# Kernel optimization log

Hardware: AMD Instinct MI355X
Metric: run time of the kernel (lower is better)

Reference implementation:

```python
import jax, jax.numpy as jnp
import numpy as np

B, H, W = 16, 512, 512
N_BINS = 511          # round(mean(shape)) - 1 for (512, 512)
MAX_R = 1.0           # (1 + min(shape)/max(shape)) / 2 for square image


def _bin_ids():
    # Precompute per-pixel radial shell index (replaces the list of boolean shell masks).
    frame = max(H, W)
    xx, yy = np.mgrid[:H, :W]
    ellipse = ((xx - H / 2) * 2 / frame) ** 2 + ((yy - W / 2) * 2 / frame) ** 2
    r2 = np.linspace(0.0, MAX_R, N_BINS + 1)[1:] ** 2
    # shell k = { r2[k-1] <= ellipse < r2[k] }; pixels with ellipse >= r2[-1] map to
    # overflow bin N_BINS and are dropped, exactly matching the xor'd ellipse masks.
    return jnp.asarray(np.searchsorted(r2, ellipse.ravel(), side='right').astype(np.int32))


BIN_IDS = _bin_ids()  # [H*W] int32 in [0, N_BINS]


def setup_inputs() -> dict:
    key = jax.random.key(0)
    k1, k2 = jax.random.split(key)
    return {
        "z_": jax.random.normal(k1, (B, H, W, 2), dtype=jnp.float32),
        "t_": jax.random.normal(k2, (B, H, W, 2), dtype=jnp.float32),
    }


def _shell_sums(x):
    # x: [B, H*W] -> per-shell sums [B, N_BINS+1] in a single fused segment-sum pass.
    return jax.vmap(lambda v: jax.ops.segment_sum(v, BIN_IDS, num_segments=N_BINS + 1))(x)


def reference(z_, t_):
    tc = t_[..., 0] + 1j * t_[..., 1]          # [B,H,W] complex target
    zc = z_[..., 0] + 1j * z_[..., 1]
    Ft = jnp.fft.fft2(tc, axes=(-2, -1))
    Fe = jnp.fft.fft2(zc - tc, axes=(-2, -1))
    norm_coeff = Ft.real ** 2 + Ft.imag ** 2   # |FFT(target)|^2, [B,H,W]
    errors = Fe.real ** 2 + Fe.imag ** 2       # |FFT(z - target)|^2
    es = _shell_sums(errors.reshape(B, -1))[:, :N_BINS]      # drop overflow bin
    ns = _shell_sums(norm_coeff.reshape(B, -1))[:, :N_BINS]
    nre = es / jnp.maximum(ns, 1e-8)           # per-batch, per-shell normed error
    # per_shell_loss = per-batch sum over shells; loss = mean over batch
    return jnp.mean(jnp.sum(nre, axis=1))
```

## Files before the change

### kernel.cpp

```cpp
#include <hip/hip_runtime.h>

#define HH 512
#define WW 512
#define NBATCH 16
#define NBINS 512
#define NREP 8

#define PI_F 3.14159265358979323846f

#define SW(r) ((r) ^ (((r) >> 4) & 0xF))
#define TSW(c, hh) (((c) << 3) + ((hh) ^ (((c) >> 1) & 7)))

#define DPP_SHR(x, n) __builtin_amdgcn_update_dpp(0, (x), 0x110 + (n), 0xF, 0xF, true)
#define DPP_SHL1(x)   __builtin_amdgcn_update_dpp(0, (x), 0x101,       0xF, 0xF, true)

__device__ __forceinline__ float2 cadd(float2 a, float2 b){ return make_float2(a.x+b.x, a.y+b.y); }
__device__ __forceinline__ float2 csub(float2 a, float2 b){ return make_float2(a.x-b.x, a.y-b.y); }
__device__ __forceinline__ float2 cmul(float2 a, float2 b){
    return make_float2(a.x*b.x - a.y*b.y, a.x*b.y + a.y*b.x);
}

__device__ __forceinline__ void dft8(const float2* a, float2* y) {
    const float s2 = 0.70710678118654752440f;
    float2 t02a = cadd(a[0], a[4]), t02s = csub(a[0], a[4]);
    float2 t13a = cadd(a[2], a[6]), t13s = csub(a[2], a[6]);
    float2 E0 = cadd(t02a, t13a);
    float2 E2 = csub(t02a, t13a);
    float2 E1 = make_float2(t02s.x + t13s.y, t02s.y - t13s.x);
    float2 E3 = make_float2(t02s.x - t13s.y, t02s.y + t13s.x);
    float2 u02a = cadd(a[1], a[5]), u02s = csub(a[1], a[5]);
    float2 u13a = cadd(a[3], a[7]), u13s = csub(a[3], a[7]);
    float2 O0 = cadd(u02a, u13a);
    float2 O2 = csub(u02a, u13a);
    float2 O1 = make_float2(u02s.x + u13s.y, u02s.y - u13s.x);
    float2 O3 = make_float2(u02s.x - u13s.y, u02s.y + u13s.x);
    float2 wO1 = make_float2(s2 * (O1.x + O1.y), s2 * (O1.y - O1.x));
    float2 wO2 = make_float2(O2.y, -O2.x);
    float2 wO3 = make_float2(s2 * (O3.y - O3.x), -s2 * (O3.x + O3.y));
    y[0] = cadd(E0, O0);  y[4] = csub(E0, O0);
    y[1] = cadd(E1, wO1); y[5] = csub(E1, wO1);
    y[2] = cadd(E2, wO2); y[6] = csub(E2, wO2);
    y[3] = cadd(E3, wO3); y[7] = csub(E3, wO3);
}

__device__ __forceinline__ void twiddle8(float base, float2* w) {
    float s1, c1, s4, c4;
    __sincosf(base, &s1, &c1);
    __sincosf(4.0f * base, &s4, &c4);
    w[0] = make_float2(1.0f, 0.0f);
    w[1] = make_float2(c1, s1);
    w[2] = cmul(w[1], w[1]);
    w[3] = cmul(w[2], w[1]);
    w[4] = make_float2(c4, s4);
    w[5] = cmul(w[4], w[1]);
    w[6] = cmul(w[4], w[2]);
    w[7] = cmul(w[4], w[3]);
}

__device__ __forceinline__ void fft512_stage0_store(float2* rb, int lane, const float2* a) {
    float2 y[8]; dft8(a, y);
    float2 w[8]; twiddle8(-PI_F * (float)lane * (1.0f / 256.0f), w);
#pragma unroll
    for (int r = 0; r < 8; ++r) rb[SW(8 * lane + r)] = cmul(y[r], w[r]);
}

__device__ __forceinline__ void fft512_stage1(float2* rb, int lane) {
    float2 a[8];
#pragma unroll
    for (int u = 0; u < 8; ++u) a[u] = rb[SW(lane + 64 * u)];
    float2 y[8]; dft8(a, y);
    float2 w[8]; twiddle8(-PI_F * (float)(lane >> 3) * (1.0f / 32.0f), w);
    const int qb = (lane & 7) + ((lane >> 3) << 6);
#pragma unroll
    for (int r = 0; r < 8; ++r) rb[SW(qb + 8 * r)] = cmul(y[r], w[r]);
}

__device__ __forceinline__ void fft512_stage2(const float2* rb, int lane, float2* y) {
    float2 a[8];
#pragma unroll
    for (int u = 0; u < 8; ++u) a[u] = rb[SW(lane + 64 * u)];
    dft8(a, y);
}

__global__ __launch_bounds__(512, 4)
void row_fft_kernel(const float2* __restrict__ z, const float2* __restrict__ t,
                    float2* __restrict__ fieldsT, int b0) {
    __shared__ float2 buf[8 * 512];
    const int tid  = threadIdx.x;
    const int lane = tid & 63;
    const int g    = tid >> 6;
    const int bid  = blockIdx.x;
    const int hg   = bid & 63;
    const int lb   = bid >> 6;
    const int b    = b0 + lb;
    const int h    = (hg << 3) | g;
    const size_t rowOff = ((size_t)(b * HH + h)) * WW;

    const float2* tr = t + rowOff;
    const float2* zr = z + rowOff;
    float2 tv[8], zv[8];
#pragma unroll
    for (int u = 0; u < 8; ++u) tv[u] = tr[lane + 64 * u];
#pragma unroll
    for (int u = 0; u < 8; ++u) zv[u] = zr[lane + 64 * u];

    float2* rb = buf + (g << 9);
#pragma unroll
    for (int f = 0; f < 2; ++f) {
        float2 a[8];
        if (f == 0) {
#pragma unroll
            for (int u = 0; u < 8; ++u) a[u] = tv[u];
        } else {
#pragma unroll
            for (int u = 0; u < 8; ++u) a[u] = make_float2(zv[u].x - tv[u].x,
                                                           zv[u].y - tv[u].y);
        }
        fft512_stage0_store(rb, lane, a);
        __builtin_amdgcn_wave_barrier();
        fft512_stage1(rb, lane);
        __builtin_amdgcn_wave_barrier();
        float2 y[8];
        fft512_stage2(rb, lane, y);

        __syncthreads();
#pragma unroll
        for (int r = 0; r < 8; ++r) {
            int c = lane + (r << 6);
            buf[TSW(c, g)] = y[r];
        }
        __syncthreads();
        float2* outF = fieldsT + ((size_t)(lb * 2 + f) << 18);
#pragma unroll
        for (int k = 0; k < 8; ++k) {
            int e  = tid + (k << 9);
            int c  = e >> 3;
            int hh = e & 7;
            outF[((size_t)c << 9) + (hg << 3) + hh] = buf[TSW(c, hh)];
        }
        __syncthreads();
    }
}

__global__ __launch_bounds__(256, 8)
void col_fft_bin_kernel(const float2* __restrict__ fieldsT,
                        float* __restrict__ binsR, int b0) {
    __shared__ float2 buf[4 * 512];
    const int tid  = threadIdx.x;
    const int lane = tid & 63;
    const int g    = tid >> 6;
    const int bid  = blockIdx.x;
    const int cq   = bid & 127;
    const int f    = (bid >> 7) & 1;
    const int lb   = bid >> 8;
    const int b    = b0 + lb;
    const int c    = (cq << 2) | g;

    const float2* colT = fieldsT + (((size_t)(lb * 2 + f) << 9) + c) * 512;
    float2 a[8];
#pragma unroll
    for (int u = 0; u < 8; ++u) a[u] = colT[lane + (u << 6)];

    float2* rb = buf + (g << 9);
    fft512_stage0_store(rb, lane, a);
    __builtin_amdgcn_wave_barrier();
    fft512_stage1(rb, lane);
    __builtin_amdgcn_wave_barrier();
    float2 y[8];
    fft512_stage2(rb, lane, y);
    __builtin_amdgcn_wave_barrier();
    __asm__ volatile("" ::: "memory");

#pragma unroll
    for (int j = 0; j < 4; ++j) rb[lane + (j << 6)] = make_float2(0.0f, 0.0f);
    __builtin_amdgcn_wave_barrier();
    __asm__ volatile("" ::: "memory");

    float* histw = (float*)rb;
    const int dc = c - 256;
    const unsigned fc2i = (unsigned)(dc * dc);
    const int l15 = lane & 15;
#pragma unroll
    for (int r = 0; r < 8; ++r) {
        int k  = lane + (r << 6);
        int dk = k - 256;
        unsigned m = (unsigned)(dk * dk) + fc2i;
        int bin = (int)(sqrtf((float)m) * (511.0f / 256.0f));
        unsigned long long rhs = 261121ull * (unsigned long long)m;
        unsigned bp1 = (unsigned)(bin + 1);
        if (((unsigned long long)(bp1 * bp1) << 16) <= rhs) ++bin;
        else if (((unsigned long long)((unsigned)bin * (unsigned)bin) << 16) > rhs) --bin;
        bin = (m < 65536u) ? bin : 511;

        float v = y[r].x * y[r].x + y[r].y * y[r].y;

        int nb; float nv;
        nb = DPP_SHR(bin, 1);
        nv = __int_as_float(DPP_SHR(__float_as_int(v), 1));
        v += (l15 >= 1 && nb == bin) ? nv : 0.0f;
        nb = DPP_SHR(bin, 2);
        nv = __int_as_float(DPP_SHR(__float_as_int(v), 2));
        v += (l15 >= 2 && nb == bin) ? nv : 0.0f;
        nb = DPP_SHR(bin, 4);
        nv = __int_as_float(DPP_SHR(__float_as_int(v), 4));
        v += (l15 >= 4 && nb == bin) ? nv : 0.0f;
        nb = DPP_SHR(bin, 8);
        nv = __int_as_float(DPP_SHR(__float_as_int(v), 8));
        v += (l15 >= 8 && nb == bin) ? nv : 0.0f;

        int nxt = DPP_SHL1(bin);
        if (l15 == 15 || nxt != bin)
            atomicAdd(&histw[bin], v);
    }
    __syncthreads();

    const float* bufF = (const float*)buf;
    float s0 = 0.0f, s1 = 0.0f;
#pragma unroll
    for (int w = 0; w < 4; ++w) {
        s0 += bufF[(w << 10) + tid];
        s1 += bufF[(w << 10) + 256 + tid];
    }
    const int fl = f * NBATCH + b;
    float* dst = binsR + ((size_t)(bid & (NREP - 1)) * 2 * NBATCH + fl) * NBINS;
    atomicAdd(&dst[tid], s0);
    atomicAdd(&dst[tid + 256], s1);
}

__global__ __launch_bounds__(512)
void reduce_bins_kernel(const float* __restrict__ binsR, float* __restrict__ bins) {
    const int tid = threadIdx.x;
    const int fl  = blockIdx.x;
    float s = 0.0f;
#pragma unroll
    for (int x = 0; x < NREP; ++x)
        s += binsR[((size_t)x * 2 * NBATCH + fl) * NBINS + tid];
    bins[(size_t)fl * NBINS + tid] = s;
}

__global__ __launch_bounds__(512)
void loss_kernel(const float* __restrict__ bins, float* __restrict__ outp) {
    __shared__ float red[512];
    const int tid = threadIdx.x;
    float acc = 0.0f;
    if (tid < 511) {
#pragma unroll 4
        for (int b = 0; b < NBATCH; ++b) {
            float ns = bins[((size_t)b) * NBINS + tid];
            float es = bins[((size_t)(NBATCH + b)) * NBINS + tid];
            acc += es / fmaxf(ns, 1e-8f);
        }
    }
    red[tid] = acc;
    __syncthreads();
    for (int s = 256; s > 0; s >>= 1) {
        if (tid < s) red[tid] += red[tid + s];
        __syncthreads();
    }
    if (tid == 0) outp[0] = red[0] * (1.0f / NBATCH);
}

extern "C" void kernel_launch(void* const* d_in, const int* in_sizes, int n_in,
                              void* d_out, int out_size, void* d_ws, size_t ws_size,
                              hipStream_t stream) {
    const float2* z = (const float2*)d_in[0];
    const float2* t = (const float2*)d_in[1];
    float* outp = (float*)d_out;

    const size_t binsRBytes = (size_t)NREP * 2 * NBATCH * NBINS * sizeof(float);
    const size_t binsBytes  = (size_t)2 * NBATCH * NBINS * sizeof(float);
    const size_t fixedBytes = binsRBytes + binsBytes;
    const size_t fpb = (size_t)2 * HH * WW * sizeof(float2);

    int CB = 16;
    while (CB > 1 && fixedBytes + (size_t)CB * fpb > ws_size) CB >>= 1;

    float*  binsR   = (float*)d_ws;
    float*  bins    = (float*)((char*)d_ws + binsRBytes);
    float2* fieldsT = (float2*)((char*)d_ws + fixedBytes);

    hipMemsetAsync(binsR, 0, binsRBytes, stream);

    for (int b0 = 0; b0 < NBATCH; b0 += CB) {
        row_fft_kernel<<<CB * 64, 512, 0, stream>>>(z, t, fieldsT, b0);
        col_fft_bin_kernel<<<CB * 2 * 128, 256, 0, stream>>>(fieldsT, binsR, b0);
    }
    reduce_bins_kernel<<<32, 512, 0, stream>>>(binsR, bins);
    loss_kernel<<<1, 512, 0, stream>>>(bins, outp);
}
```

Baseline: 160.2 us.

## Interleave column pairs in transposed buffer and replace bin atomics with partial stores

The row FFT now writes its transposed output with two adjacent columns interleaved, so each column-FFT load reads 16-byte pairs with a stride. The goal is to improve write coalescing in the row kernel. The column kernel no longer does global atomicAdds into 8 replica histograms. Each of the 128 column-quad blocks writes its own partial histogram, which the reduce kernel then sums, so the memset can go. The cost is a larger partials buffer and a 128-deep reduction per bin, and the column loads now use stride-2 float2 accesses.

```diff
diff --git a/kernel.cpp b/kernel.cpp
--- a/kernel.cpp
+++ b/kernel.cpp
@@ -4,7 +4,7 @@
 #define WW 512
 #define NBATCH 16
 #define NBINS 512
-#define NREP 8
+#define NCQ 128
 
 #define PI_F 3.14159265358979323846f
 
@@ -136,7 +136,8 @@
             int e  = tid + (k << 9);
             int c  = e >> 3;
             int hh = e & 7;
-            outF[((size_t)c << 9) + (hg << 3) + hh] = buf[TSW(c, hh)];
+            int hr = (hg << 3) | hh;
+            outF[((size_t)(c >> 1) << 10) + (hr << 1) + (c & 1)] = buf[TSW(c, hh)];
         }
         __syncthreads();
     }
@@ -144,22 +145,23 @@
 
 __global__ __launch_bounds__(256, 8)
 void col_fft_bin_kernel(const float2* __restrict__ fieldsT,
-                        float* __restrict__ binsR, int b0) {
+                        float* __restrict__ partials, int b0) {
     __shared__ float2 buf[4 * 512];
     const int tid  = threadIdx.x;
     const int lane = tid & 63;
     const int g    = tid >> 6;
     const int bid  = blockIdx.x;
-    const int cq   = bid & 127;
+    const int cq   = bid & (NCQ - 1);
     const int f    = (bid >> 7) & 1;
     const int lb   = bid >> 8;
     const int b    = b0 + lb;
     const int c    = (cq << 2) | g;
 
-    const float2* colT = fieldsT + (((size_t)(lb * 2 + f) << 9) + c) * 512;
+    const float2* colT = fieldsT + ((size_t)(lb * 2 + f) << 18)
+                                 + ((size_t)(c >> 1) << 10) + (c & 1);
     float2 a[8];
 #pragma unroll
-    for (int u = 0; u < 8; ++u) a[u] = colT[lane + (u << 6)];
+    for (int u = 0; u < 8; ++u) a[u] = colT[(lane + (u << 6)) << 1];
 
     float2* rb = buf + (g << 9);
     fft512_stage0_store(rb, lane, a);
@@ -222,19 +224,19 @@
         s1 += bufF[(w << 10) + 256 + tid];
     }
     const int fl = f * NBATCH + b;
-    float* dst = binsR + ((size_t)(bid & (NREP - 1)) * 2 * NBATCH + fl) * NBINS;
-    atomicAdd(&dst[tid], s0);
-    atomicAdd(&dst[tid + 256], s1);
+    float* dst = partials + ((size_t)(cq << 5) + (size_t)fl) * NBINS;
+    dst[tid] = s0;
+    dst[tid + 256] = s1;
 }
 
 __global__ __launch_bounds__(512)
-void reduce_bins_kernel(const float* __restrict__ binsR, float* __restrict__ bins) {
+void reduce_bins_kernel(const float* __restrict__ partials, float* __restrict__ bins) {
     const int tid = threadIdx.x;
     const int fl  = blockIdx.x;
     float s = 0.0f;
-#pragma unroll
-    for (int x = 0; x < NREP; ++x)
-        s += binsR[((size_t)x * 2 * NBATCH + fl) * NBINS + tid];
+#pragma unroll 8
+    for (int cq = 0; cq < NCQ; ++cq)
+        s += partials[((size_t)(cq << 5) + fl) * NBINS + tid];
     bins[(size_t)fl * NBINS + tid] = s;
 }
 
@@ -267,24 +269,22 @@
     const float2* t = (const float2*)d_in[1];
     float* outp = (float*)d_out;
 
-    const size_t binsRBytes = (size_t)NREP * 2 * NBATCH * NBINS * sizeof(float);
-    const size_t binsBytes  = (size_t)2 * NBATCH * NBINS * sizeof(float);
-    const size_t fixedBytes = binsRBytes + binsBytes;
+    const size_t partialsBytes = (size_t)NCQ * 2 * NBATCH * NBINS * sizeof(float);
+    const size_t binsBytes     = (size_t)2 * NBATCH * NBINS * sizeof(float);
+    const size_t fixedBytes    = partialsBytes + binsBytes;
     const size_t fpb = (size_t)2 * HH * WW * sizeof(float2);
 
     int CB = 16;
     while (CB > 1 && fixedBytes + (size_t)CB * fpb > ws_size) CB >>= 1;
 
-    float*  binsR   = (float*)d_ws;
-    float*  bins    = (float*)((char*)d_ws + binsRBytes);
-    float2* fieldsT = (float2*)((char*)d_ws + fixedBytes);
-
-    hipMemsetAsync(binsR, 0, binsRBytes, stream);
+    float*  partials = (float*)d_ws;
+    float*  bins     = (float*)((char*)d_ws + partialsBytes);
+    float2* fieldsT  = (float2*)((char*)d_ws + fixedBytes);
 
     for (int b0 = 0; b0 < NBATCH; b0 += CB) {
         row_fft_kernel<<<CB * 64, 512, 0, stream>>>(z, t, fieldsT, b0);
-        col_fft_bin_kernel<<<CB * 2 * 128, 256, 0, stream>>>(fieldsT, binsR, b0);
-    }
-    reduce_bins_kernel<<<32, 512, 0, stream>>>(binsR, bins);
+        col_fft_bin_kernel<<<CB * 2 * NCQ, 256, 0, stream>>>(fieldsT, partials, b0);
+    }
+    reduce_bins_kernel<<<32, 512, 0, stream>>>(partials, bins);
     loss_kernel<<<1, 512, 0, stream>>>(bins, outp);
 }
```

Measured after the change: 157.7 us. No clear change (-1.6%).
